# Optimization experiments

Hardware: AMD Instinct MI355X
Metric: run time of the kernel (lower is better)

The kernel has to match this reference:

```python
import jax, jax.numpy as jnp
import numpy as np

DIM = 384
HEADS = 12
WS = 7


def setup_inputs() -> dict:
    key = jax.random.key(0)
    ks = jax.random.split(key, 5)
    B, H, W = 16, 56, 56
    x = jax.random.normal(ks[0], (B, H * W, DIM), dtype=jnp.float32)
    # torch Linear weight (out,in) used as x @ W here, qkv_bias=False
    w_qkv = jax.random.normal(ks[1], (DIM, 3 * DIM), dtype=jnp.float32) * 0.02
    w_proj = jax.random.normal(ks[2], (DIM, DIM), dtype=jnp.float32) * 0.02
    b_proj = jax.random.normal(ks[3], (DIM,), dtype=jnp.float32) * 0.02
    # depthwise 3x3 conv (groups=dim): HWIO kernel (3,3,1,DIM), bias=True
    w_conv = jax.random.normal(ks[4], (3, 3, 1, DIM), dtype=jnp.float32) * 0.02
    b_conv = jnp.zeros((DIM,), jnp.float32)
    return {"x": x, "w_qkv": w_qkv, "w_proj": w_proj, "b_proj": b_proj,
            "w_conv": w_conv, "b_conv": b_conv, "H": H, "W": W}


def reference(x, w_qkv, w_proj, b_proj, w_conv, b_conv, H, W):
    B, N, C = x.shape
    hd = C // HEADS
    scale = hd ** (-0.5)
    hg, wg = H // WS, W // WS  # H,W chosen divisible by ws (no-pad fast path)

    qkv = x @ w_qkv  # (B, N, 3C)
    q, k, v = jnp.split(qkv, 3, axis=-1)

    def to_win(t):
        # (B,N,C) -> (B, n_windows, heads, ws*ws, head_dim)
        t = t.reshape(B, hg, WS, wg, WS, HEADS, hd)
        return t.transpose(0, 1, 3, 5, 2, 4, 6).reshape(B, hg * wg, HEADS, WS * WS, hd)

    qw, kw, vw = to_win(q), to_win(k), to_win(v)

    attn = jax.nn.softmax(jnp.einsum('bwhqd,bwhkd->bwhqk', qw, kw) * scale, axis=-1)
    out = jnp.einsum('bwhqk,bwhkd->bwhqd', attn, vw)
    # merge windows back: (B,nw,heads,q,d) -> (B,N,C)
    out = out.reshape(B, hg, wg, HEADS, WS, WS, hd)
    out = out.transpose(0, 1, 4, 2, 5, 3, 6).reshape(B, N, C)

    # LIM: win2img(img2win(v)) is just v as (B,C,H,W); depthwise 3x3 conv
    v_img = v.reshape(B, H, W, C).transpose(0, 3, 1, 2)
    v_lim = jax.lax.conv_general_dilated(
        v_img, w_conv, window_strides=(1, 1), padding='SAME',
        dimension_numbers=('NCHW', 'HWIO', 'NCHW'), feature_group_count=C)
    v_lim = v_lim + b_conv[None, :, None, None]
    v_lim = v_lim.reshape(B, C, N).transpose(0, 2, 1)  # (B, N, C)

    out = out + v_lim
    return out @ w_proj + b_proj
```

## Files before the change

### kernel.cpp

```cpp
#include <hip/hip_runtime.h>
#include <cstdint>
#include <cstddef>

typedef __bf16 bf16x8 __attribute__((ext_vector_type(8)));
typedef float floatx4 __attribute__((ext_vector_type(4)));

#define DEV static __device__ __forceinline__

DEV float bf2f(uint16_t u) {
    union { uint32_t i; float f; } x; x.i = ((uint32_t)u) << 16; return x.f;
}
DEV uint16_t f2bf(float f) {
    uint32_t u = __float_as_uint(f);
    uint32_t r = (u + 0x7FFFu + ((u >> 16) & 1u)) >> 16;
    return (uint16_t)r;
}
DEV bf16x8 as_bf8(uint4 u) {
    union { uint4 u; bf16x8 b; } c; c.u = u; return c.b;
}
DEV void g2l16(const void* g, void* l) {
    __builtin_amdgcn_global_load_lds(
        (const __attribute__((address_space(1))) void*)g,
        (__attribute__((address_space(3))) void*)l, 16, 0, 0);
}

union U16x8 { uint16_t h[8]; uint4 u; };

constexpr int DIMC  = 384;
constexpr int HEADS = 12;
constexpr int IMH   = 56, IMW = 56;
constexpr int NTOK  = IMH * IMW;
constexpr int BATCH = 16;
constexpr int MTOT  = BATCH * NTOK;
constexpr int QKVLD = 3 * DIMC;
constexpr int GK    = 384;

__global__ __launch_bounds__(256) void cvt_bf16(const float* __restrict__ in,
                                                uint16_t* __restrict__ out)
{
    size_t i = ((size_t)blockIdx.x * 256 + threadIdx.x) * 8;
    float4 a = *(const float4*)(in + i);
    float4 b = *(const float4*)(in + i + 4);
    U16x8 t;
    t.h[0] = f2bf(a.x); t.h[1] = f2bf(a.y); t.h[2] = f2bf(a.z); t.h[3] = f2bf(a.w);
    t.h[4] = f2bf(b.x); t.h[5] = f2bf(b.y); t.h[6] = f2bf(b.z); t.h[7] = f2bf(b.w);
    *(uint4*)(out + i) = t.u;
}

__global__ __launch_bounds__(256) void transpose_cvt(const float* __restrict__ in,
                                                     uint16_t* __restrict__ out,
                                                     int R, int C)
{
    int idx = blockIdx.x * 256 + threadIdx.x;
    int r = idx % R, c = idx / R;
    out[idx] = f2bf(in[(size_t)r * C + c]);
}

template<bool CF32>
__global__ __launch_bounds__(256) void gemm_bt(const uint16_t* __restrict__ A,
                                               const uint16_t* __restrict__ Bt,
                                               const float* __restrict__ bias,
                                               void* __restrict__ Cptr,
                                               int N)
{
    __shared__ __align__(16) uint16_t sA[2][128 * 32];
    __shared__ __align__(16) uint16_t sB[2][128 * 32];

    const int t    = threadIdx.x;
    const int NB   = N >> 7;
    const int bid  = blockIdx.x;
    const int chunk = bid / (8 * NB);
    const int r     = bid % (8 * NB);
    const int bm    = chunk * 8 + (r & 7);
    const int bn    = r >> 3;
    const int wave = t >> 6, lane = t & 63;
    const int wm   = (wave >> 1) * 64, wn = (wave & 1) * 64;
    const int lr   = lane & 15, quad = lane >> 4;

    const uint16_t* Ag = A  + (size_t)(bm * 128 + (t >> 2)) * GK + (t & 3) * 8;
    const uint16_t* Bg = Bt + (size_t)(bn * 128 + (t >> 2)) * GK + (t & 3) * 8;

    auto stage = [&](int buf, int k0) {
        g2l16(Ag + k0, sA[buf] + wave * 512);
        g2l16(Ag + (size_t)64 * GK + k0, sA[buf] + 2048 + wave * 512);
        g2l16(Bg + k0, sB[buf] + wave * 512);
        g2l16(Bg + (size_t)64 * GK + k0, sB[buf] + 2048 + wave * 512);
    };

    floatx4 acc[4][4] = {};

    stage(0, 0);
    __syncthreads();

    #pragma unroll
    for (int ks = 0; ks < 12; ++ks) {
        const int cur = ks & 1;
        if (ks < 11) stage(cur ^ 1, (ks + 1) * 32);

        bf16x8 af[4], bfr[4];
        #pragma unroll
        for (int mt = 0; mt < 4; ++mt)
            af[mt] = *(const bf16x8*)&sA[cur][(wm + mt * 16 + lr) * 32 + quad * 8];
        #pragma unroll
        for (int nt = 0; nt < 4; ++nt)
            bfr[nt] = *(const bf16x8*)&sB[cur][(wn + nt * 16 + lr) * 32 + quad * 8];
        #pragma unroll
        for (int mt = 0; mt < 4; ++mt)
            #pragma unroll
            for (int nt = 0; nt < 4; ++nt)
                acc[mt][nt] = __builtin_amdgcn_mfma_f32_16x16x32_bf16(
                    af[mt], bfr[nt], acc[mt][nt], 0, 0, 0);

        __syncthreads();
    }

    #pragma unroll
    for (int mt = 0; mt < 4; ++mt) {
        #pragma unroll
        for (int nt = 0; nt < 4; ++nt) {
            int gc = bn * 128 + wn + nt * 16 + lr;
            float bv = bias ? bias[gc] : 0.0f;
            int gr0 = bm * 128 + wm + mt * 16 + quad * 4;
            #pragma unroll
            for (int i = 0; i < 4; ++i) {
                if constexpr (CF32) {
                    ((float*)Cptr)[(size_t)(gr0 + i) * N + gc] = acc[mt][nt][i] + bv;
                } else {
                    ((uint16_t*)Cptr)[(size_t)(gr0 + i) * N + gc] = f2bf(acc[mt][nt][i] + bv);
                }
            }
        }
    }
}

constexpr int PLD = 72;
constexpr int WAVE_ELEMS = 32 * PLD + 81 * 32;

__global__ __launch_bounds__(128) void attn_mfma(const uint16_t* __restrict__ qkv,
                                                 const float* __restrict__ wconv,
                                                 const float* __restrict__ bconv,
                                                 uint16_t* __restrict__ y)
{
    __shared__ uint16_t lds[2][WAVE_ELEMS];
    __shared__ float    warr_all[2][320];

    const int wave = threadIdx.x >> 6;
    const int lane = threadIdx.x & 63;
    const int unit = blockIdx.x * 2 + wave;
    const int h  = unit % HEADS;
    const int w  = (unit / HEADS) & 63;
    const int b  = unit / (HEADS * 64);
    const int wy = w >> 3, wx = w & 7;
    const int lr = lane & 15, quad = lane >> 4;

    uint16_t* Vt    = lds[wave];
    uint16_t* Vhalo = lds[wave] + 32 * PLD;
    float*    warr  = warr_all[wave];

    #pragma unroll
    for (int it = 0; it < 5; ++it) {
        int idx = it * 64 + lane;
        if (idx < 288) warr[idx] = wconv[(idx >> 5) * DIMC + h * 32 + (idx & 31)];
    }
    if (lane < 32) warr[288 + lane] = bconv[h * 32 + lane];

    #pragma unroll
    for (int it = 0; it < 6; ++it) {
        int u = it * 16 + (lane >> 2);
        int g = lane & 3;
        if (u < 81) {
            int hy = u / 9, hx = u % 9;
            int iy = wy * 7 + hy - 1, ix = wx * 7 + hx - 1;
            uint4 val{0, 0, 0, 0};
            if (iy >= 0 && iy < IMH && ix >= 0 && ix < IMW)
                val = *(const uint4*)(qkv + (size_t)(b * NTOK + iy * IMW + ix) * QKVLD
                                      + 2 * DIMC + h * 32 + g * 8);
            *(uint4*)&Vhalo[u * 32 + g * 8] = val;
        }
    }

    auto rowbase = [&](int i, int which) -> const uint16_t* {
        int py = i / 7, px = i % 7;
        int n = (wy * 7 + py) * IMW + wx * 7 + px;
        return qkv + (size_t)(b * NTOK + n) * QKVLD + which * DIMC + h * 32;
    };

    uint4 qf[4], kf[4];
    #pragma unroll
    for (int tm = 0; tm < 4; ++tm) {
        int i = tm * 16 + lr;
        if (i < 49) {
            qf[tm] = *(const uint4*)(rowbase(i, 0) + quad * 8);
            kf[tm] = *(const uint4*)(rowbase(i, 1) + quad * 8);
        } else {
            qf[tm] = uint4{0, 0, 0, 0};
            kf[tm] = uint4{0, 0, 0, 0};
        }
    }

    {
        int j = lane;
        if (j < 49) {
            int hrow = (j / 7 + 1) * 9 + (j % 7 + 1);
            #pragma unroll
            for (int p = 0; p < 4; ++p) {
                U16x8 tmp; tmp.u = *(const uint4*)&Vhalo[hrow * 32 + p * 8];
                #pragma unroll
                for (int q = 0; q < 8; ++q) Vt[(p * 8 + q) * PLD + j] = tmp.h[q];
            }
        } else {
            #pragma unroll
            for (int d = 0; d < 32; ++d) Vt[d * PLD + j] = 0;
        }
    }

    floatx4 S[4][4] = {};
    #pragma unroll
    for (int ta = 0; ta < 4; ++ta)
        #pragma unroll
        for (int tb = 0; tb < 4; ++tb)
            S[ta][tb] = __builtin_amdgcn_mfma_f32_16x16x32_bf16(
                as_bf8(kf[ta]), as_bf8(qf[tb]), S[ta][tb], 0, 0, 0);

    const float scale = 0.17677669529663687f;
    float psum[4] = {0.f, 0.f, 0.f, 0.f};
    #pragma unroll
    for (int ta = 0; ta < 4; ++ta) {
        #pragma unroll
        for (int tb = 0; tb < 4; ++tb) {
            #pragma unroll
            for (int i = 0; i < 4; ++i) {
                float e;
                if (ta < 3) e = __expf(S[ta][tb][i] * scale);
                else        e = (quad == 0 && i == 0)
                                ? __expf(S[ta][tb][i] * scale) : 0.0f;
                S[ta][tb][i] = e;
                psum[tb] += e;
            }
        }
    }
    #pragma unroll
    for (int tb = 0; tb < 4; ++tb) {
        float s = psum[tb];
        s += __shfl_xor(s, 16);
        s += __shfl_xor(s, 32);
        psum[tb] = 1.0f / s;
    }

    uint32_t pkv[4][4][2];
    #pragma unroll
    for (int ta = 0; ta < 4; ++ta) {
        #pragma unroll
        for (int tb = 0; tb < 4; ++tb) {
            #pragma unroll
            for (int hh = 0; hh < 2; ++hh) {
                float lo = S[ta][tb][2 * hh]     * psum[tb];
                float hi = S[ta][tb][2 * hh + 1] * psum[tb];
                asm("v_cvt_pk_bf16_f32 %0, %1, %2"
                    : "=v"(pkv[ta][tb][hh]) : "v"(lo), "v"(hi));
            }
        }
    }

    const int lo_lane = (quad & 1) * 32 + lr;
    const bool hiq = quad >= 2;
    floatx4 Ot[2][4] = {};
    #pragma unroll
    for (int kk = 0; kk < 2; ++kk) {
        uint4 pfr[4];
        #pragma unroll
        for (int tb = 0; tb < 4; ++tb) {
            uint32_t a0 = (uint32_t)__shfl((int)pkv[kk * 2][tb][0],     lo_lane);
            uint32_t b0 = (uint32_t)__shfl((int)pkv[kk * 2 + 1][tb][0], lo_lane);
            uint32_t a1 = (uint32_t)__shfl((int)pkv[kk * 2][tb][1],     lo_lane);
            uint32_t b1 = (uint32_t)__shfl((int)pkv[kk * 2 + 1][tb][1], lo_lane);
            uint32_t a2 = (uint32_t)__shfl((int)pkv[kk * 2][tb][0],     lo_lane + 16);
            uint32_t b2 = (uint32_t)__shfl((int)pkv[kk * 2 + 1][tb][0], lo_lane + 16);
            uint32_t a3 = (uint32_t)__shfl((int)pkv[kk * 2][tb][1],     lo_lane + 16);
            uint32_t b3 = (uint32_t)__shfl((int)pkv[kk * 2 + 1][tb][1], lo_lane + 16);
            pfr[tb] = uint4{hiq ? b0 : a0, hiq ? b1 : a1,
                            hiq ? b2 : a2, hiq ? b3 : a3};
        }
        bf16x8 vf[2];
        #pragma unroll
        for (int td = 0; td < 2; ++td)
            vf[td] = *(const bf16x8*)&Vt[(td * 16 + lr) * PLD + kk * 32 + quad * 8];
        #pragma unroll
        for (int td = 0; td < 2; ++td)
            #pragma unroll
            for (int tb = 0; tb < 4; ++tb)
                Ot[td][tb] = __builtin_amdgcn_mfma_f32_16x16x32_bf16(
                    vf[td], as_bf8(pfr[tb]), Ot[td][tb], 0, 0, 0);
    }

    uint16_t* convb = Vt;
    #pragma unroll
    for (int it = 0; it < 4; ++it) {
        int u = it * 64 + lane;
        if (u < 196) {
            int j = u >> 2, g = u & 3;
            int py = j / 7, px = j % 7;
            float acc[8];
            {
                float4 b0 = *(const float4*)(warr + 288 + g * 8);
                float4 b1 = *(const float4*)(warr + 288 + g * 8 + 4);
                acc[0] = b0.x; acc[1] = b0.y; acc[2] = b0.z; acc[3] = b0.w;
                acc[4] = b1.x; acc[5] = b1.y; acc[6] = b1.z; acc[7] = b1.w;
            }
            #pragma unroll
            for (int ky = 0; ky < 3; ++ky) {
                #pragma unroll
                for (int kx = 0; kx < 3; ++kx) {
                    int hrow = (py + ky) * 9 + (px + kx);
                    U16x8 v; v.u = *(const uint4*)&Vhalo[hrow * 32 + g * 8];
                    const float* wp = warr + (ky * 3 + kx) * 32 + g * 8;
                    float4 w0 = *(const float4*)wp;
                    float4 w1 = *(const float4*)(wp + 4);
                    acc[0] += bf2f(v.h[0]) * w0.x;
                    acc[1] += bf2f(v.h[1]) * w0.y;
                    acc[2] += bf2f(v.h[2]) * w0.z;
                    acc[3] += bf2f(v.h[3]) * w0.w;
                    acc[4] += bf2f(v.h[4]) * w1.x;
                    acc[5] += bf2f(v.h[5]) * w1.y;
                    acc[6] += bf2f(v.h[6]) * w1.z;
                    acc[7] += bf2f(v.h[7]) * w1.w;
                }
            }
            U16x8 rr;
            #pragma unroll
            for (int q = 0; q < 8; ++q) rr.h[q] = f2bf(acc[q]);
            *(uint4*)&convb[j * 32 + g * 8] = rr.u;
        }
    }

    #pragma unroll
    for (int tb = 0; tb < 4; ++tb) {
        int q = tb * 16 + lr;
        if (q < 49) {
            int py = q / 7, px = q % 7;
            int n = (wy * 7 + py) * IMW + wx * 7 + px;
            uint16_t* dst = y + (size_t)(b * NTOK + n) * DIMC + h * 32;
            #pragma unroll
            for (int td = 0; td < 2; ++td) {
                int d0 = td * 16 + quad * 4;
                uint2 cv = *(const uint2*)&convb[q * 32 + d0];
                float o0 = Ot[td][tb][0] + bf2f((uint16_t)(cv.x & 0xffffu));
                float o1 = Ot[td][tb][1] + bf2f((uint16_t)(cv.x >> 16));
                float o2 = Ot[td][tb][2] + bf2f((uint16_t)(cv.y & 0xffffu));
                float o3 = Ot[td][tb][3] + bf2f((uint16_t)(cv.y >> 16));
                uint32_t w0, w1;
                asm("v_cvt_pk_bf16_f32 %0, %1, %2" : "=v"(w0) : "v"(o0), "v"(o1));
                asm("v_cvt_pk_bf16_f32 %0, %1, %2" : "=v"(w1) : "v"(o2), "v"(o3));
                *(uint2*)(dst + d0) = uint2{w0, w1};
            }
        }
    }
}

extern "C" void kernel_launch(void* const* d_in, const int* in_sizes, int n_in,
                              void* d_out, int out_size, void* d_ws, size_t ws_size,
                              hipStream_t stream)
{
    const float* x      = (const float*)d_in[0];
    const float* w_qkv  = (const float*)d_in[1];
    const float* w_proj = (const float*)d_in[2];
    const float* b_proj = (const float*)d_in[3];
    const float* w_conv = (const float*)d_in[4];
    const float* b_conv = (const float*)d_in[5];
    float* out = (float*)d_out;

    char* ws = (char*)d_ws;
    uint16_t* qkv    = (uint16_t*)ws;
    uint16_t* xb     = (uint16_t*)(ws + 115605504);
    uint16_t* yb     = xb;
    uint16_t* wqkvT  = (uint16_t*)(ws + 115605504 + 38535168);
    uint16_t* wprojT = wqkvT + QKVLD * GK;

    cvt_bf16<<<dim3((MTOT * DIMC) / (8 * 256)), 256, 0, stream>>>(x, xb);
    transpose_cvt<<<dim3((GK * QKVLD) / 256), 256, 0, stream>>>(w_qkv, wqkvT, GK, QKVLD);
    transpose_cvt<<<dim3((GK * DIMC) / 256), 256, 0, stream>>>(w_proj, wprojT, GK, DIMC);

    gemm_bt<false><<<dim3((MTOT / 128) * (QKVLD / 128)), 256, 0, stream>>>(
        xb, wqkvT, nullptr, qkv, QKVLD);

    attn_mfma<<<dim3(BATCH * 64 * HEADS / 2), 128, 0, stream>>>(
        qkv, w_conv, b_conv, yb);

    gemm_bt<true><<<dim3((MTOT / 128) * (DIMC / 128)), 256, 0, stream>>>(
        yb, wprojT, b_proj, out, DIMC);
}
```

Measured before the change: 307.5 us.

## Enlarge GEMM tiles to 256x128 with 8 waves and merge prep kernels

Both GEMMs now use 512-thread blocks covering 256x128 output tiles, which halves B-tile reloads per output and raises MFMA work per barrier. The M-tile grid is padded to 200 so the grouping of 8 M-tiles divides evenly; padded blocks compute on rows past the end of A and skip their stores. The bf16 conversion of x and the two weight-transpose conversions are folded into one launch to cut launch overhead. The out-of-range padded reads depend on the workspace memory that follows the A buffer.

```diff
diff --git a/kernel.cpp b/kernel.cpp
--- a/kernel.cpp
+++ b/kernel.cpp
@@ -34,36 +34,46 @@
 constexpr int MTOT  = BATCH * NTOK;
 constexpr int QKVLD = 3 * DIMC;
 constexpr int GK    = 384;
-
-__global__ __launch_bounds__(256) void cvt_bf16(const float* __restrict__ in,
-                                                uint16_t* __restrict__ out)
+constexpr int MTILES_PAD = 200;
+
+constexpr int CVTB  = (MTOT * DIMC) / (8 * 256);
+constexpr int TQKVB = (GK * QKVLD) / 256;
+constexpr int TPRJB = (GK * DIMC) / 256;
+
+__global__ __launch_bounds__(256) void prep_kernel(
+    const float* __restrict__ x,      uint16_t* __restrict__ xb,
+    const float* __restrict__ w_qkv,  uint16_t* __restrict__ wqkvT,
+    const float* __restrict__ w_proj, uint16_t* __restrict__ wprojT)
 {
-    size_t i = ((size_t)blockIdx.x * 256 + threadIdx.x) * 8;
-    float4 a = *(const float4*)(in + i);
-    float4 b = *(const float4*)(in + i + 4);
-    U16x8 t;
-    t.h[0] = f2bf(a.x); t.h[1] = f2bf(a.y); t.h[2] = f2bf(a.z); t.h[3] = f2bf(a.w);
-    t.h[4] = f2bf(b.x); t.h[5] = f2bf(b.y); t.h[6] = f2bf(b.z); t.h[7] = f2bf(b.w);
-    *(uint4*)(out + i) = t.u;
-}
-
-__global__ __launch_bounds__(256) void transpose_cvt(const float* __restrict__ in,
-                                                     uint16_t* __restrict__ out,
-                                                     int R, int C)
-{
-    int idx = blockIdx.x * 256 + threadIdx.x;
-    int r = idx % R, c = idx / R;
-    out[idx] = f2bf(in[(size_t)r * C + c]);
+    int bid = blockIdx.x;
+    int t   = threadIdx.x;
+    if (bid < CVTB) {
+        size_t i = ((size_t)bid * 256 + t) * 8;
+        float4 a = *(const float4*)(x + i);
+        float4 b = *(const float4*)(x + i + 4);
+        U16x8 o;
+        o.h[0] = f2bf(a.x); o.h[1] = f2bf(a.y); o.h[2] = f2bf(a.z); o.h[3] = f2bf(a.w);
+        o.h[4] = f2bf(b.x); o.h[5] = f2bf(b.y); o.h[6] = f2bf(b.z); o.h[7] = f2bf(b.w);
+        *(uint4*)(xb + i) = o.u;
+    } else if (bid < CVTB + TQKVB) {
+        int idx = (bid - CVTB) * 256 + t;
+        int r = idx % GK, c = idx / GK;
+        wqkvT[idx] = f2bf(w_qkv[(size_t)r * QKVLD + c]);
+    } else {
+        int idx = (bid - CVTB - TQKVB) * 256 + t;
+        int r = idx % GK, c = idx / GK;
+        wprojT[idx] = f2bf(w_proj[(size_t)r * DIMC + c]);
+    }
 }
 
 template<bool CF32>
-__global__ __launch_bounds__(256) void gemm_bt(const uint16_t* __restrict__ A,
+__global__ __launch_bounds__(512) void gemm_bt(const uint16_t* __restrict__ A,
                                                const uint16_t* __restrict__ Bt,
                                                const float* __restrict__ bias,
                                                void* __restrict__ Cptr,
                                                int N)
 {
-    __shared__ __align__(16) uint16_t sA[2][128 * 32];
+    __shared__ __align__(16) uint16_t sA[2][256 * 32];
     __shared__ __align__(16) uint16_t sB[2][128 * 32];
 
     const int t    = threadIdx.x;
@@ -74,17 +84,18 @@
     const int bm    = chunk * 8 + (r & 7);
     const int bn    = r >> 3;
     const int wave = t >> 6, lane = t & 63;
-    const int wm   = (wave >> 1) * 64, wn = (wave & 1) * 64;
+    const int wm   = (wave >> 1) * 64;
+    const int wn   = (wave & 1) * 64;
     const int lr   = lane & 15, quad = lane >> 4;
-
-    const uint16_t* Ag = A  + (size_t)(bm * 128 + (t >> 2)) * GK + (t & 3) * 8;
+    const bool mvalid = (bm * 256 + 256) <= MTOT;
+
+    const uint16_t* Ag = A  + (size_t)(bm * 256 + (t >> 2)) * GK + (t & 3) * 8;
     const uint16_t* Bg = Bt + (size_t)(bn * 128 + (t >> 2)) * GK + (t & 3) * 8;
 
     auto stage = [&](int buf, int k0) {
         g2l16(Ag + k0, sA[buf] + wave * 512);
-        g2l16(Ag + (size_t)64 * GK + k0, sA[buf] + 2048 + wave * 512);
+        g2l16(Ag + (size_t)128 * GK + k0, sA[buf] + 4096 + wave * 512);
         g2l16(Bg + k0, sB[buf] + wave * 512);
-        g2l16(Bg + (size_t)64 * GK + k0, sB[buf] + 2048 + wave * 512);
     };
 
     floatx4 acc[4][4] = {};
@@ -114,13 +125,15 @@
         __syncthreads();
     }
 
+    if (!mvalid) return;
+
     #pragma unroll
     for (int mt = 0; mt < 4; ++mt) {
         #pragma unroll
         for (int nt = 0; nt < 4; ++nt) {
             int gc = bn * 128 + wn + nt * 16 + lr;
             float bv = bias ? bias[gc] : 0.0f;
-            int gr0 = bm * 128 + wm + mt * 16 + quad * 4;
+            int gr0 = bm * 256 + wm + mt * 16 + quad * 4;
             #pragma unroll
             for (int i = 0; i < 4; ++i) {
                 if constexpr (CF32) {
@@ -376,16 +389,15 @@
     uint16_t* wqkvT  = (uint16_t*)(ws + 115605504 + 38535168);
     uint16_t* wprojT = wqkvT + QKVLD * GK;
 
-    cvt_bf16<<<dim3((MTOT * DIMC) / (8 * 256)), 256, 0, stream>>>(x, xb);
-    transpose_cvt<<<dim3((GK * QKVLD) / 256), 256, 0, stream>>>(w_qkv, wqkvT, GK, QKVLD);
-    transpose_cvt<<<dim3((GK * DIMC) / 256), 256, 0, stream>>>(w_proj, wprojT, GK, DIMC);
-
-    gemm_bt<false><<<dim3((MTOT / 128) * (QKVLD / 128)), 256, 0, stream>>>(
+    prep_kernel<<<dim3(CVTB + TQKVB + TPRJB), 256, 0, stream>>>(
+        x, xb, w_qkv, wqkvT, w_proj, wprojT);
+
+    gemm_bt<false><<<dim3(MTILES_PAD * (QKVLD / 128)), 512, 0, stream>>>(
         xb, wqkvT, nullptr, qkv, QKVLD);
 
     attn_mfma<<<dim3(BATCH * 64 * HEADS / 2), 128, 0, stream>>>(
         qkv, w_conv, b_conv, yb);
 
-    gemm_bt<true><<<dim3((MTOT / 128) * (DIMC / 128)), 256, 0, stream>>>(
+    gemm_bt<true><<<dim3(MTILES_PAD * (DIMC / 128)), 512, 0, stream>>>(
         yb, wprojT, b_proj, out, DIMC);
 }
```

Result: faster. 300.9 us (-2.2%).
